# Kernel tuning notes

Measured on AMD Instinct MI355X. Metric: run time of the kernel, lower is better.

## Reference

```python
import jax, jax.numpy as jnp
import numpy as np
from jax import lax

DN = ('NCH', 'OIH', 'NCH')

def _conv(x, w, b, pad):
    # x: [B, C, L]; replication (edge) pad then VALID conv, per nn.ReplicationPad1d + Conv1d
    if pad != (0, 0):
        x = jnp.pad(x, ((0, 0), (0, 0), pad), mode='edge')
    y = lax.conv_general_dilated(x, w, (1,), 'VALID', dimension_numbers=DN)
    return y + b[None, :, None]

def setup_inputs() -> dict:
    key = jax.random.key(0)
    ks = jax.random.split(key, 11)
    B, L, C, H = 32, 512, 300, 512
    s = 1.0 / np.sqrt(C)
    inp = {
        'x': jax.random.normal(ks[0], (B, L, C), jnp.float32),
        'w1': jax.random.normal(ks[1], (C, C, 1), jnp.float32) * s,
        'b1': jax.random.normal(ks[2], (C,), jnp.float32) * s,
        'w2': jax.random.normal(ks[3], (C, C, 2), jnp.float32) * s,
        'b2': jax.random.normal(ks[4], (C,), jnp.float32) * s,
        'w3': jax.random.normal(ks[5], (C, C, 3), jnp.float32) * s,
        'b3': jax.random.normal(ks[6], (C,), jnp.float32) * s,
        'w7': jax.random.normal(ks[7], (C, C, 7), jnp.float32) * s,
        'b7': jax.random.normal(ks[8], (C,), jnp.float32) * s,
        'slp_w': jax.random.normal(ks[9], (H, 5 * C), jnp.float32) * (1.0 / np.sqrt(5 * C)),
        'slp_b': jax.random.normal(ks[10], (H,), jnp.float32) * (1.0 / np.sqrt(5 * C)),
    }
    return inp

def reference(x, w1, b1, w2, b2, w3, b3, w7, b7, slp_w, slp_b):
    xc = jnp.transpose(x, (0, 2, 1))  # [B, C, L]
    x1 = jnp.tanh(_conv(xc, w1, b1, (0, 0)))
    x2 = jnp.tanh(_conv(xc, w2, b2, (0, 1)))
    x3 = jnp.tanh(_conv(xc, w3, b3, (1, 1)))
    x5 = x3  # faithful to the original bug: x5 = self.conv3(x)
    x7 = jnp.tanh(_conv(xc, w7, b7, (3, 3)))
    # concat channels -> [B, L, 1500], then linear + tanh -> [B, L, 512]
    h = jnp.concatenate([x1, x2, x3, x5, x7], axis=1)  # [B, 5C, L]
    h = jnp.transpose(h, (0, 2, 1))  # [B, L, 5C]
    out = jnp.tanh(jnp.einsum('blc,hc->blh', h, slp_w) + slp_b)
    return out
```

## Files before the change

kernel.cpp:

```cpp
#include <hip/hip_runtime.h>
#include <hip/hip_bf16.h>

typedef __attribute__((ext_vector_type(8))) short short8;
typedef __attribute__((ext_vector_type(16))) float floatx16;

#define Bn 32
#define Ln 512
#define Cn 300
#define Hn 512
#define Nn (Bn*Ln)
#define XBP 518
#define XBC 320
#define HK 1216
#define LDSTC 72

#define XROWS 134
#define XSZ (XROWS*LDSTC)
#define HSROWS 128
#define HSSZ (HSROWS*LDSTC)

#define XB_ELEMS (Bn*XBP*XBC)
#define WB_ELEMS 1597440
#define WC_ELEMS (Hn*HK)
#define XB_OFF 0
#define WB_OFF (XB_OFF + XB_ELEMS)
#define WC_OFF (WB_OFF + WB_ELEMS)
#define HB_OFF (WC_OFF + WC_ELEMS)

__device__ __forceinline__ float fast_tanh(float x) {
    float ax = __builtin_fabsf(x);
    float t  = __expf(-2.f * ax);
    float r  = __builtin_fmaf(-2.f * t, __frcp_rn(1.f + t), 1.f);
    return __builtin_copysignf(r, x);
}

__global__ void prep_all(const float* __restrict__ x,
                         const float* __restrict__ w1, const float* __restrict__ w2,
                         const float* __restrict__ w3, const float* __restrict__ w7,
                         const float* __restrict__ slp_w,
                         __hip_bfloat16* __restrict__ wsb) {
    int idx = blockIdx.x * 256 + threadIdx.x;
    if (idx < XB_ELEMS) {
        int c = idx % XBC;
        int t = idx / XBC;
        int p = t % XBP;
        int b = t / XBP;
        int l = p - 3;
        l = l < 0 ? 0 : (l > Ln - 1 ? Ln - 1 : l);
        float v = (c < Cn) ? x[(b * Ln + l) * Cn + c] : 0.f;
        wsb[idx] = __float2bfloat16(v);
    } else if (idx < WB_OFF + WB_ELEMS) {
        int r = idx - WB_OFF, taps; const float* w;
        if (r < 122880)       { taps = 1; w = w1; }
        else if (r < 368640)  { taps = 2; w = w2; r -= 122880; }
        else if (r < 737280)  { taps = 3; w = w3; r -= 368640; }
        else                  { taps = 7; w = w7; r -= 737280; }
        int e    = r & 7;
        int lane = (r >> 3) & 63;
        int f    = (r >> 9) & 15;
        int rt   = r >> 13;
        int t    = rt % taps;
        int mc   = rt / taps;
        int ch   = mc % 5;
        int mt   = mc / 5;
        int ks = f >> 2, mq = f & 3;
        int m = mt * 128 + mq * 32 + (lane & 31);
        int c = ch * 64 + ks * 16 + (lane >> 5) * 8 + e;
        float v = (m < Cn && c < Cn) ? w[(m * Cn + c) * taps + t] : 0.f;
        wsb[idx] = __float2bfloat16(v);
    } else if (idx < WC_OFF + WC_ELEMS) {
        int r = idx - WC_OFF;
        int e    = r & 7;
        int lane = (r >> 3) & 63;
        int f    = (r >> 9) & 15;
        int mc   = r >> 13;
        int ch   = mc % 19;
        int mt4  = mc / 19;
        int ks = f >> 2, mq = f & 3;
        int h = mt4 * 128 + mq * 32 + (lane & 31);
        int k = ch * 64 + ks * 16 + (lane >> 5) * 8 + e;
        const float* row = slp_w + h * 1500;
        float v;
        if (k < 600)       v = row[k];
        else if (k < 900)  v = row[k] + row[k + 300];
        else if (k < 1200) v = row[k + 300];
        else               v = 0.f;
        wsb[idx] = __float2bfloat16(v);
    }
}

#define MFMA __builtin_amdgcn_mfma_f32_32x32x16_bf16

template<int TAPS, int LEAD>
__device__ __forceinline__ void conv_body(
        const short* __restrict__ xbs, const short* __restrict__ wsp,
        const float* __restrict__ bias, int cid, int mt, int nt,
        __hip_bfloat16* __restrict__ hbuf, short* xs) {
    const int tid  = threadIdx.x;
    const int lane = tid & 63;
    const int wave = tid >> 6;
    const int wn = wave & 1, wm = wave >> 1;
    const int lr = lane & 31;
    const int lk = (lane >> 5) << 3;
    const int TRIG = (TAPS >= 3) ? TAPS - 2 : 0;

    floatx16 acc[2][2];
#pragma unroll
    for (int i = 0; i < 2; i++)
#pragma unroll
        for (int j = 0; j < 2; j++)
#pragma unroll
            for (int r = 0; r < 16; r++) acc[i][j][r] = 0.f;

    short8 bA[8], bB[8], st[5];

#pragma unroll
    for (int i = 0; i < 5; ++i) {
        int j = tid + 256 * i;
        if (i < 4 || j < 1072)
            st[i] = *(const short8*)&xbs[(j >> 3) * XBC + ((j & 7) << 3)];
    }
#pragma unroll
    for (int ks = 0; ks < 4; ++ks)
#pragma unroll
        for (int mf = 0; mf < 2; ++mf)
            bA[ks * 2 + mf] = *(const short8*)&wsp[(ks * 4 + wm * 2 + mf) * 512 + lane * 8];
#pragma unroll
    for (int i = 0; i < 5; ++i) {
        int j = tid + 256 * i;
        if (i < 4 || j < 1072)
            *(short8*)&xs[(j >> 3) * LDSTC + ((j & 7) << 3)] = st[i];
    }
    __syncthreads();

    for (int c5 = 0; c5 < 5; ++c5) {
        const short* cur = xs + (c5 & 1) * XSZ;
        short* nxt = xs + ((c5 + 1) & 1) * XSZ;
        const int c0n = (c5 + 1) * 64;
#pragma unroll
        for (int t = 0; t < TAPS; ++t) {
            if (!(c5 == 4 && t == TAPS - 1)) {
                const short* wtn = (t + 1 < TAPS) ? wsp + (c5 * TAPS + t + 1) * 8192
                                                  : wsp + ((c5 + 1) * TAPS) * 8192;
#pragma unroll
                for (int ks = 0; ks < 4; ++ks)
#pragma unroll
                    for (int mf = 0; mf < 2; ++mf)
                        bB[ks * 2 + mf] = *(const short8*)&wtn[(ks * 4 + wm * 2 + mf) * 512 + lane * 8];
            }
            if (t == TRIG && c5 < 4) {
#pragma unroll
                for (int i = 0; i < 5; ++i) {
                    int j = tid + 256 * i;
                    if (i < 4 || j < 1072)
                        st[i] = *(const short8*)&xbs[(j >> 3) * XBC + c0n + ((j & 7) << 3)];
                }
            }
            const int sh = t - LEAD + 3;
            const int ar = (wn * 64 + lr + sh) * LDSTC + lk;
#pragma unroll
            for (int ks = 0; ks < 4; ++ks) {
                short8 a0 = *(const short8*)&cur[ar + ks * 16];
                short8 a1 = *(const short8*)&cur[ar + 32 * LDSTC + ks * 16];
                acc[0][0] = MFMA(a0, bA[ks * 2 + 0], acc[0][0], 0, 0, 0);
                acc[0][1] = MFMA(a0, bA[ks * 2 + 1], acc[0][1], 0, 0, 0);
                acc[1][0] = MFMA(a1, bA[ks * 2 + 0], acc[1][0], 0, 0, 0);
                acc[1][1] = MFMA(a1, bA[ks * 2 + 1], acc[1][1], 0, 0, 0);
            }
            if (!(c5 == 4 && t == TAPS - 1)) {
#pragma unroll
                for (int f = 0; f < 8; ++f) bA[f] = bB[f];
            }
        }
        if (c5 < 4) {
#pragma unroll
            for (int i = 0; i < 5; ++i) {
                int j = tid + 256 * i;
                if (i < 4 || j < 1072)
                    *(short8*)&nxt[(j >> 3) * LDSTC + ((j & 7) << 3)] = st[i];
            }
        }
        __syncthreads();
    }

#pragma unroll
    for (int mi = 0; mi < 2; ++mi) {
        int mloc = mt * 128 + wm * 64 + mi * 32 + lr;
        if (mloc < Cn) {
            float bv = bias[mloc];
            int col = cid * Cn + mloc;
#pragma unroll
            for (int ni = 0; ni < 2; ++ni) {
                floatx16 v = acc[ni][mi];
#pragma unroll
                for (int reg = 0; reg < 16; ++reg) {
                    int nl = wn * 64 + ni * 32 + (reg & 3) + ((reg >> 2) << 3) + ((lane >> 5) << 2);
                    int n = nt * 128 + nl;
                    hbuf[n * HK + col] = __float2bfloat16(fast_tanh(v[reg] + bv));
                }
            }
        }
    }
}

__global__ __launch_bounds__(256, 2) void conv_kernel(
        const __hip_bfloat16* __restrict__ xbg, const __hip_bfloat16* __restrict__ Wbg,
        const float* __restrict__ bias1, const float* __restrict__ bias2,
        const float* __restrict__ bias3, const float* __restrict__ bias7,
        __hip_bfloat16* __restrict__ hbuf) {
    __shared__ __align__(16) short xs[2 * XSZ];

    const int nt = blockIdx.x;
    const int my = blockIdx.y;
    const int g  = my / 3;
    const int mt = my % 3;

    const int b  = nt >> 2;
    const int l0 = (nt & 3) << 7;
    const short* xbs = (const short*)xbg + (b * XBP + l0) * XBC;
    const short* wb  = (const short*)Wbg;

    if (g == 0)      conv_body<7, 3>(xbs, wb + 737280 + mt * 7 * 40960, bias7, 3, mt, nt, hbuf, xs);
    else if (g == 1) conv_body<3, 1>(xbs, wb + 368640 + mt * 3 * 40960, bias3, 2, mt, nt, hbuf, xs);
    else if (g == 2) conv_body<2, 0>(xbs, wb + 122880 + mt * 2 * 40960, bias2, 1, mt, nt, hbuf, xs);
    else             conv_body<1, 0>(xbs, wb +      0 + mt * 1 * 40960, bias1, 0, mt, nt, hbuf, xs);
}

__global__ __launch_bounds__(256, 2) void linear_kernel(
        const __hip_bfloat16* __restrict__ hbufg, const __hip_bfloat16* __restrict__ Wcg,
        const float* __restrict__ slp_b, float* __restrict__ out) {
    __shared__ __align__(16) short hs[2 * HSSZ];

    const int tid  = threadIdx.x;
    const int lane = tid & 63;
    const int wave = tid >> 6;
    const int wn = wave & 1, wm = wave >> 1;
    const int lr = lane & 31;
    const int lk = (lane >> 5) << 3;

    const int nt  = blockIdx.x;
    const int mt4 = blockIdx.y;

    const short* hbp = (const short*)hbufg + nt * 128 * HK;
    const short* wcp = (const short*)Wcg + mt4 * 155648;

    const int srow = tid >> 1;
    const int scc  = (tid & 1) << 5;
    floatx16 acc[2][2];
#pragma unroll
    for (int i = 0; i < 2; i++)
#pragma unroll
        for (int j = 0; j < 2; j++)
#pragma unroll
            for (int r = 0; r < 16; r++) acc[i][j][r] = 0.f;

    short8 bA[8], bB[8], st[4];
    (void)srow; (void)scc;

#pragma unroll
    for (int i = 0; i < 4; ++i) {
        int j = tid + 256 * i;
        st[i] = *(const short8*)&hbp[(j >> 3) * HK + ((j & 7) << 3)];
    }
#pragma unroll
    for (int ks = 0; ks < 4; ++ks)
#pragma unroll
        for (int mf = 0; mf < 2; ++mf)
            bA[ks * 2 + mf] = *(const short8*)&wcp[(ks * 4 + wm * 2 + mf) * 512 + lane * 8];
#pragma unroll
    for (int i = 0; i < 4; ++i) {
        int j = tid + 256 * i;
        *(short8*)&hs[(j >> 3) * LDSTC + ((j & 7) << 3)] = st[i];
    }
    __syncthreads();

    for (int ch = 0; ch < 19; ++ch) {
        const short* cur = hs + (ch & 1) * HSSZ;
        short* nxt = hs + ((ch + 1) & 1) * HSSZ;
        if (ch < 18) {
            const short* wtn = wcp + (ch + 1) * 8192;
#pragma unroll
            for (int ks = 0; ks < 4; ++ks)
#pragma unroll
                for (int mf = 0; mf < 2; ++mf)
                    bB[ks * 2 + mf] = *(const short8*)&wtn[(ks * 4 + wm * 2 + mf) * 512 + lane * 8];
            const int c0n = (ch + 1) * 64;
#pragma unroll
            for (int i = 0; i < 4; ++i) {
                int j = tid + 256 * i;
                st[i] = *(const short8*)&hbp[(j >> 3) * HK + c0n + ((j & 7) << 3)];
            }
        }
        const int ar = (wn * 64 + lr) * LDSTC + lk;
#pragma unroll
        for (int ks = 0; ks < 4; ++ks) {
            short8 a0 = *(const short8*)&cur[ar + ks * 16];
            short8 a1 = *(const short8*)&cur[ar + 32 * LDSTC + ks * 16];
            acc[0][0] = MFMA(a0, bA[ks * 2 + 0], acc[0][0], 0, 0, 0);
            acc[0][1] = MFMA(a0, bA[ks * 2 + 1], acc[0][1], 0, 0, 0);
            acc[1][0] = MFMA(a1, bA[ks * 2 + 0], acc[1][0], 0, 0, 0);
            acc[1][1] = MFMA(a1, bA[ks * 2 + 1], acc[1][1], 0, 0, 0);
        }
        if (ch < 18) {
#pragma unroll
            for (int f = 0; f < 8; ++f) bA[f] = bB[f];
#pragma unroll
            for (int i = 0; i < 4; ++i) {
                int j = tid + 256 * i;
                *(short8*)&nxt[(j >> 3) * LDSTC + ((j & 7) << 3)] = st[i];
            }
        }
        __syncthreads();
    }

#pragma unroll
    for (int mi = 0; mi < 2; ++mi) {
        int h = mt4 * 128 + wm * 64 + mi * 32 + lr;
        float bv = slp_b[h];
#pragma unroll
        for (int ni = 0; ni < 2; ++ni) {
            floatx16 v = acc[ni][mi];
#pragma unroll
            for (int reg = 0; reg < 16; ++reg) {
                int nl = wn * 64 + ni * 32 + (reg & 3) + ((reg >> 2) << 3) + ((lane >> 5) << 2);
                int n = nt * 128 + nl;
                out[n * Hn + h] = fast_tanh(v[reg] + bv);
            }
        }
    }
}


extern "C" void kernel_launch(void* const* d_in, const int* in_sizes, int n_in,
                              void* d_out, int out_size, void* d_ws, size_t ws_size,
                              hipStream_t stream) {
    const float* x     = (const float*)d_in[0];
    const float* w1    = (const float*)d_in[1];
    const float* b1    = (const float*)d_in[2];
    const float* w2    = (const float*)d_in[3];
    const float* b2    = (const float*)d_in[4];
    const float* w3    = (const float*)d_in[5];
    const float* b3    = (const float*)d_in[6];
    const float* w7    = (const float*)d_in[7];
    const float* b7    = (const float*)d_in[8];
    const float* slp_w = (const float*)d_in[9];
    const float* slp_b = (const float*)d_in[10];

    __hip_bfloat16* wsb = (__hip_bfloat16*)d_ws;

    const int prep_total = XB_ELEMS + WB_ELEMS + WC_ELEMS;
    prep_all<<<(prep_total + 255) / 256, 256, 0, stream>>>(x, w1, w2, w3, w7, slp_w, wsb);

    conv_kernel<<<dim3(128, 12), 256, 0, stream>>>(wsb + XB_OFF, wsb + WB_OFF,
                                                   b1, b2, b3, b7, wsb + HB_OFF);
    linear_kernel<<<dim3(128, 4), 256, 0, stream>>>(wsb + HB_OFF, wsb + WC_OFF,
                                                    slp_b, (float*)d_out);
}
```

Before: 191.3 us.

## Vectorize prep by 8, pair conv branches per block, zero-fill hbuf padding

```diff
diff --git a/kernel.cpp b/kernel.cpp
--- a/kernel.cpp
+++ b/kernel.cpp
@@ -34,28 +34,46 @@
     return __builtin_copysignf(r, x);
 }
 
+__device__ __forceinline__ short f2bf(float v) {
+    __hip_bfloat16 h = __float2bfloat16(v);
+    return *reinterpret_cast<short*>(&h);
+}
+
 __global__ void prep_all(const float* __restrict__ x,
                          const float* __restrict__ w1, const float* __restrict__ w2,
                          const float* __restrict__ w3, const float* __restrict__ w7,
                          const float* __restrict__ slp_w,
                          __hip_bfloat16* __restrict__ wsb) {
-    int idx = blockIdx.x * 256 + threadIdx.x;
+    int g = blockIdx.x * 256 + threadIdx.x;
+    int idx = g * 8;
+    short8 o;
     if (idx < XB_ELEMS) {
-        int c = idx % XBC;
-        int t = idx / XBC;
+        int c8 = idx % XBC;
+        int t  = idx / XBC;
         int p = t % XBP;
         int b = t / XBP;
         int l = p - 3;
         l = l < 0 ? 0 : (l > Ln - 1 ? Ln - 1 : l);
-        float v = (c < Cn) ? x[(b * Ln + l) * Cn + c] : 0.f;
-        wsb[idx] = __float2bfloat16(v);
+        const float* row = x + (b * Ln + l) * Cn;
+        if (c8 + 8 <= Cn) {
+            float4 a = *(const float4*)(row + c8);
+            float4 bq = *(const float4*)(row + c8 + 4);
+            o[0] = f2bf(a.x); o[1] = f2bf(a.y); o[2] = f2bf(a.z); o[3] = f2bf(a.w);
+            o[4] = f2bf(bq.x); o[5] = f2bf(bq.y); o[6] = f2bf(bq.z); o[7] = f2bf(bq.w);
+        } else {
+#pragma unroll
+            for (int e = 0; e < 8; ++e) {
+                int c = c8 + e;
+                o[e] = f2bf(c < Cn ? row[c] : 0.f);
+            }
+        }
+        *(short8*)&wsb[idx] = o;
     } else if (idx < WB_OFF + WB_ELEMS) {
         int r = idx - WB_OFF, taps; const float* w;
         if (r < 122880)       { taps = 1; w = w1; }
         else if (r < 368640)  { taps = 2; w = w2; r -= 122880; }
         else if (r < 737280)  { taps = 3; w = w3; r -= 368640; }
         else                  { taps = 7; w = w7; r -= 737280; }
-        int e    = r & 7;
         int lane = (r >> 3) & 63;
         int f    = (r >> 9) & 15;
         int rt   = r >> 13;
@@ -65,12 +83,15 @@
         int mt   = mc / 5;
         int ks = f >> 2, mq = f & 3;
         int m = mt * 128 + mq * 32 + (lane & 31);
-        int c = ch * 64 + ks * 16 + (lane >> 5) * 8 + e;
-        float v = (m < Cn && c < Cn) ? w[(m * Cn + c) * taps + t] : 0.f;
-        wsb[idx] = __float2bfloat16(v);
+        int cb = ch * 64 + ks * 16 + (lane >> 5) * 8;
+#pragma unroll
+        for (int e = 0; e < 8; ++e) {
+            int c = cb + e;
+            o[e] = f2bf((m < Cn && c < Cn) ? w[(m * Cn + c) * taps + t] : 0.f);
+        }
+        *(short8*)&wsb[idx] = o;
     } else if (idx < WC_OFF + WC_ELEMS) {
         int r = idx - WC_OFF;
-        int e    = r & 7;
         int lane = (r >> 3) & 63;
         int f    = (r >> 9) & 15;
         int mc   = r >> 13;
@@ -78,14 +99,19 @@
         int mt4  = mc / 19;
         int ks = f >> 2, mq = f & 3;
         int h = mt4 * 128 + mq * 32 + (lane & 31);
-        int k = ch * 64 + ks * 16 + (lane >> 5) * 8 + e;
+        int kb = ch * 64 + ks * 16 + (lane >> 5) * 8;
         const float* row = slp_w + h * 1500;
-        float v;
-        if (k < 600)       v = row[k];
-        else if (k < 900)  v = row[k] + row[k + 300];
-        else if (k < 1200) v = row[k + 300];
-        else               v = 0.f;
-        wsb[idx] = __float2bfloat16(v);
+#pragma unroll
+        for (int e = 0; e < 8; ++e) {
+            int k = kb + e;
+            float v;
+            if (k < 600)       v = row[k];
+            else if (k < 900)  v = row[k] + row[k + 300];
+            else if (k < 1200) v = row[k + 300];
+            else               v = 0.f;
+            o[e] = f2bf(v);
+        }
+        *(short8*)&wsb[idx] = o;
     }
 }
 
@@ -186,9 +212,9 @@
 #pragma unroll
     for (int mi = 0; mi < 2; ++mi) {
         int mloc = mt * 128 + wm * 64 + mi * 32 + lr;
+        int col = cid * Cn + mloc;
         if (mloc < Cn) {
             float bv = bias[mloc];
-            int col = cid * Cn + mloc;
 #pragma unroll
             for (int ni = 0; ni < 2; ++ni) {
                 floatx16 v = acc[ni][mi];
@@ -199,11 +225,21 @@
                     hbuf[n * HK + col] = __float2bfloat16(fast_tanh(v[reg] + bv));
                 }
             }
-        }
-    }
-}
-
-__global__ __launch_bounds__(256, 2) void conv_kernel(
+        } else if (cid == 3 && col < HK) {
+            __hip_bfloat16 z = __float2bfloat16(0.f);
+#pragma unroll
+            for (int ni = 0; ni < 2; ++ni)
+#pragma unroll
+                for (int reg = 0; reg < 16; ++reg) {
+                    int nl = wn * 64 + ni * 32 + (reg & 3) + ((reg >> 2) << 3) + ((lane >> 5) << 2);
+                    int n = nt * 128 + nl;
+                    hbuf[n * HK + col] = z;
+                }
+        }
+    }
+}
+
+__global__ __launch_bounds__(256, 3) void conv_kernel(
         const __hip_bfloat16* __restrict__ xbg, const __hip_bfloat16* __restrict__ Wbg,
         const float* __restrict__ bias1, const float* __restrict__ bias2,
         const float* __restrict__ bias3, const float* __restrict__ bias7,
@@ -211,19 +247,21 @@
     __shared__ __align__(16) short xs[2 * XSZ];
 
     const int nt = blockIdx.x;
-    const int my = blockIdx.y;
-    const int g  = my / 3;
-    const int mt = my % 3;
+    const int y  = blockIdx.y;
+    const int mt = (y >= 3) ? y - 3 : y;
 
     const int b  = nt >> 2;
     const int l0 = (nt & 3) << 7;
     const short* xbs = (const short*)xbg + (b * XBP + l0) * XBC;
     const short* wb  = (const short*)Wbg;
 
-    if (g == 0)      conv_body<7, 3>(xbs, wb + 737280 + mt * 7 * 40960, bias7, 3, mt, nt, hbuf, xs);
-    else if (g == 1) conv_body<3, 1>(xbs, wb + 368640 + mt * 3 * 40960, bias3, 2, mt, nt, hbuf, xs);
-    else if (g == 2) conv_body<2, 0>(xbs, wb + 122880 + mt * 2 * 40960, bias2, 1, mt, nt, hbuf, xs);
-    else             conv_body<1, 0>(xbs, wb +      0 + mt * 1 * 40960, bias1, 0, mt, nt, hbuf, xs);
+    if (y < 3) {
+        conv_body<7, 3>(xbs, wb + 737280 + mt * 7 * 40960, bias7, 3, mt, nt, hbuf, xs);
+        conv_body<1, 0>(xbs, wb +          mt * 1 * 40960, bias1, 0, mt, nt, hbuf, xs);
+    } else {
+        conv_body<3, 1>(xbs, wb + 368640 + mt * 3 * 40960, bias3, 2, mt, nt, hbuf, xs);
+        conv_body<2, 0>(xbs, wb + 122880 + mt * 2 * 40960, bias2, 1, mt, nt, hbuf, xs);
+    }
 }
 
 __global__ __launch_bounds__(256, 2) void linear_kernel(
@@ -244,8 +282,6 @@
     const short* hbp = (const short*)hbufg + nt * 128 * HK;
     const short* wcp = (const short*)Wcg + mt4 * 155648;
 
-    const int srow = tid >> 1;
-    const int scc  = (tid & 1) << 5;
     floatx16 acc[2][2];
 #pragma unroll
     for (int i = 0; i < 2; i++)
@@ -255,7 +291,6 @@
             for (int r = 0; r < 16; r++) acc[i][j][r] = 0.f;
 
     short8 bA[8], bB[8], st[4];
-    (void)srow; (void)scc;
 
 #pragma unroll
     for (int i = 0; i < 4; ++i) {
@@ -348,11 +383,11 @@
 
     __hip_bfloat16* wsb = (__hip_bfloat16*)d_ws;
 
-    const int prep_total = XB_ELEMS + WB_ELEMS + WC_ELEMS;
-    prep_all<<<(prep_total + 255) / 256, 256, 0, stream>>>(x, w1, w2, w3, w7, slp_w, wsb);
-
-    conv_kernel<<<dim3(128, 12), 256, 0, stream>>>(wsb + XB_OFF, wsb + WB_OFF,
-                                                   b1, b2, b3, b7, wsb + HB_OFF);
+    const int prep_groups = (XB_ELEMS + WB_ELEMS + WC_ELEMS) / 8;
+    prep_all<<<(prep_groups + 255) / 256, 256, 0, stream>>>(x, w1, w2, w3, w7, slp_w, wsb);
+
+    conv_kernel<<<dim3(128, 6), 256, 0, stream>>>(wsb + XB_OFF, wsb + WB_OFF,
+                                                  b1, b2, b3, b7, wsb + HB_OFF);
     linear_kernel<<<dim3(128, 4), 256, 0, stream>>>(wsb + HB_OFF, wsb + WC_OFF,
                                                     slp_b, (float*)d_out);
 }
```

Result: slower. 216.4 us (+13.1%).
